# Performance work log

Hardware: AMD Instinct MI355X
Metric: run time of the kernel (lower is better)

## Reference

```python
import jax, jax.numpy as jnp
import numpy as np

DIM, N_HEADS, N_KV_HEADS = 2048, 32, 8
HEAD_DIM = DIM // N_HEADS            # 64
KV_REPEAT = N_HEADS // N_KV_HEADS    # 4
ROPE_THETA = 10000.0


def _rope(x, start_pos):
    # x: [B, T, Hx, hd]  (rotate-half / GPT-NeoX style RoPE)
    B, T, Hx, hd = x.shape
    half = hd // 2
    inv_freq = 1.0 / (ROPE_THETA ** (jnp.arange(half, dtype=jnp.float32) / half))
    pos = (start_pos + jnp.arange(T)).astype(jnp.float32)
    ang = pos[:, None] * inv_freq[None, :]            # [T, half]
    cos = jnp.cos(ang)[None, :, None, :]              # [1, T, 1, half]
    sin = jnp.sin(ang)[None, :, None, :]
    x1, x2 = x[..., :half], x[..., half:]
    return jnp.concatenate([x1 * cos - x2 * sin, x1 * sin + x2 * cos], axis=-1).astype(x.dtype)


def setup_inputs() -> dict:
    key = jax.random.key(0)
    ks = jax.random.split(key, 5)
    B, T = 2, 2048
    s = 1.0 / np.sqrt(DIM)
    return {
        "x": jax.random.normal(ks[0], (B, T, DIM), dtype=jnp.float32),
        "Wq": jax.random.normal(ks[1], (DIM, N_HEADS * HEAD_DIM), dtype=jnp.float32) * s,
        "Wk": jax.random.normal(ks[2], (DIM, N_KV_HEADS * HEAD_DIM), dtype=jnp.float32) * s,
        "Wv": jax.random.normal(ks[3], (DIM, N_KV_HEADS * HEAD_DIM), dtype=jnp.float32) * s,
        "Wo": jax.random.normal(ks[4], (DIM, DIM), dtype=jnp.float32) * s,
        "start_pos": 0,
    }


def reference(x, Wq, Wk, Wv, Wo, start_pos):
    B, T, _ = x.shape
    G, R, hd = N_KV_HEADS, KV_REPEAT, HEAD_DIM
    # projections -> [B, T, H, hd]
    Q = (x @ Wq).reshape(B, T, N_HEADS, hd)
    K = (x @ Wk).reshape(B, T, G, hd)
    V = (x @ Wv).reshape(B, T, G, hd)
    Q = _rope(Q, start_pos)
    K = _rope(K, start_pos)
    # GQA: group query heads as (G kv-groups, R repeats) matching repeat_interleave order
    Qg = Q.reshape(B, T, G, R, hd)
    scale = 1.0 / jnp.sqrt(jnp.asarray(hd, dtype=Q.dtype))
    scores = jnp.einsum('bqgrd,bkgd->bgrqk', Qg, K) * scale   # [B,G,R,T,T]
    # causal mask (is_causal=True since T > 1)
    causal = jnp.tril(jnp.ones((T, T), dtype=bool))
    scores = jnp.where(causal[None, None, None, :, :], scores, jnp.finfo(scores.dtype).min)
    attn = jax.nn.softmax(scores, axis=-1)
    out = jnp.einsum('bgrqk,bkgd->bqgrd', attn, V).reshape(B, T, DIM)
    y = out @ Wo
    # original also returns (K, V) with heads-first layout [B, G, T, hd]
    return (y, K.transpose(0, 2, 1, 3), V.transpose(0, 2, 1, 3))
```

## Files before the change

kernel.cpp:

```cpp
#include <hip/hip_runtime.h>
#include <hip/hip_bf16.h>
#include <stdint.h>


typedef __attribute__((ext_vector_type(4))) float f32x4;
typedef __attribute__((ext_vector_type(16))) float f32x16;
typedef __attribute__((ext_vector_type(8))) short sfrag;
typedef __attribute__((ext_vector_type(8))) __bf16 bfrag;
typedef __attribute__((ext_vector_type(4))) unsigned int u32x4;
typedef unsigned short u16;

__device__ __forceinline__ f32x4 mfma16(sfrag a, sfrag b, f32x4 c) {
  return __builtin_amdgcn_mfma_f32_16x16x32_bf16(
      __builtin_bit_cast(bfrag, a), __builtin_bit_cast(bfrag, b), c, 0, 0, 0);
}
__device__ __forceinline__ f32x16 mfma32(sfrag a, sfrag b, f32x16 c) {
  return __builtin_amdgcn_mfma_f32_32x32x16_bf16(
      __builtin_bit_cast(bfrag, a), __builtin_bit_cast(bfrag, b), c, 0, 0, 0);
}
__device__ __forceinline__ u16 f2b(float f) {
  return __builtin_bit_cast(u16, (__bf16)f);
}
__device__ __forceinline__ unsigned pack2(float a, float b) {
  return (unsigned)f2b(a) | ((unsigned)f2b(b) << 16);
}
__device__ __forceinline__ void swap32(unsigned& a, unsigned& b) {
  asm("v_permlane32_swap_b32 %0, %1" : "+v"(a), "+v"(b));
}

#define GAS __attribute__((address_space(1)))
#define LAS __attribute__((address_space(3)))
__device__ __forceinline__ void gll16(const void* g, void* l) {
  __builtin_amdgcn_global_load_lds((GAS unsigned int*)g, (LAS unsigned int*)l, 16, 0, 0);
}

__global__ __launch_bounds__(256) void k_convx(const float* __restrict__ X,
                                               u16* __restrict__ Y,
                                               const int* __restrict__ sp,
                                               float2* __restrict__ csn) {
  const int bid = blockIdx.x;
  if (bid < 8192) {
    const int i = (bid * 256 + threadIdx.x) * 4;
    float4 v = *(const float4*)(X + i);
    *(ushort4*)(Y + i) = make_ushort4(f2b(v.x), f2b(v.y), f2b(v.z), f2b(v.w));
  } else {
    const int i = (bid - 8192) * 256 + threadIdx.x;
    const int t = i >> 5, j = i & 31;
    const float freq = powf(10000.0f, -(float)j * (1.0f / 32.0f));
    const float ang = (float)(sp[0] + t) * freq;
    csn[i] = make_float2(cosf(ang), sinf(ang));
  }
}

__global__ __launch_bounds__(256) void k_convTall(const float* __restrict__ Wq,
                                                  const float* __restrict__ Wk,
                                                  const float* __restrict__ Wv,
                                                  const float* __restrict__ Wo,
                                                  u16* __restrict__ Wqkvt,
                                                  u16* __restrict__ Wot) {
  __shared__ float tile[64][65];
  const int bx = blockIdx.x;
  const int k0 = blockIdx.y * 64;
  const float* W; int N, n0; u16* Dst; int nd;
  if (bx < 32)      { W = Wq; N = 2048; n0 = bx * 64;        Dst = Wqkvt; nd = n0; }
  else if (bx < 40) { W = Wk; N = 512;  n0 = (bx - 32) * 64; Dst = Wqkvt; nd = 2048 + n0; }
  else if (bx < 48) { W = Wv; N = 512;  n0 = (bx - 40) * 64; Dst = Wqkvt; nd = 2560 + n0; }
  else              { W = Wo; N = 2048; n0 = (bx - 48) * 64; Dst = Wot;   nd = n0; }
  const int tid = threadIdx.x;
  #pragma unroll
  for (int it = 0; it < 4; ++it) {
    const int idx = it * 256 + tid;
    const int kk = idx >> 4, nq = idx & 15;
    float4 v = *(const float4*)(W + (size_t)(k0 + kk) * N + n0 + nq * 4);
    tile[kk][nq * 4 + 0] = v.x;
    tile[kk][nq * 4 + 1] = v.y;
    tile[kk][nq * 4 + 2] = v.z;
    tile[kk][nq * 4 + 3] = v.w;
  }
  __syncthreads();
  #pragma unroll
  for (int it = 0; it < 4; ++it) {
    const int idx = it * 256 + tid;
    const int nn = idx >> 4, kq = idx & 15;
    ushort4 o;
    o.x = f2b(tile[kq * 4 + 0][nn]);
    o.y = f2b(tile[kq * 4 + 1][nn]);
    o.z = f2b(tile[kq * 4 + 2][nn]);
    o.w = f2b(tile[kq * 4 + 3][nn]);
    *(ushort4*)(Dst + (size_t)(nd + nn) * 2048 + k0 + kq * 4) = o;
  }
}

__global__ __launch_bounds__(512, 2) void k_gemmQKV(const u16* __restrict__ A,
                                                    const u16* __restrict__ Bt,
                                                    int K, int GY,
                                                    const float2* __restrict__ csn,
                                                    u16* __restrict__ Qb,
                                                    u16* __restrict__ Kb,
                                                    float* __restrict__ Kout,
                                                    float* __restrict__ Vout) {
  __shared__ u16 lds[16384];
  char* const L = (char*)&lds[0];
  const int tid = threadIdx.x;
  const int q8 = gridDim.x >> 3;
  const int id2 = (blockIdx.x & 7) * q8 + (blockIdx.x >> 3);
  const int by = id2 % GY, bx = id2 / GY;
  const int wid = tid >> 6, lane = tid & 63;
  const int wm = wid >> 1, wn = wid & 1;
  const int l16 = lane & 15, l4 = lane >> 4;
  const size_t K2 = (size_t)K * 2;
  const char* Ab = (const char*)(A + (size_t)(by * 128) * K);
  const char* Bb = (const char*)(Bt + (size_t)(bx * 128) * K);
  const int NT = K >> 6;

  auto stage = [&](const char* gb, int reg, int t) {
    #pragma unroll
    for (int rd = 0; rd < 2; ++rd) {
      const int p = rd * 8192 + tid * 16;
      const int r = p >> 7;
      const int cb = (p & 127) ^ ((r & 7) << 4);
      gll16(gb + (size_t)r * K2 + (size_t)t * 128 + cb, L + reg + p);
    }
  };

  const int swz = (l16 & 7) << 4;
  const int c0 = (l4 * 16) ^ swz;
  const int c1 = (64 + l4 * 16) ^ swz;
  const int aOff = (wm * 32 + l16) * 128;
  const int bOff = 16384 + (wn * 64 + l16) * 128;

  f32x4 acc[2][4];
  #pragma unroll
  for (int m = 0; m < 2; ++m)
    #pragma unroll
    for (int n = 0; n < 4; ++n) acc[m][n] = f32x4{0.f, 0.f, 0.f, 0.f};

  for (int t = 0; t < NT; ++t) {
    stage(Ab, 0, t);
    stage(Bb, 16384, t);
    __syncthreads();
    sfrag a0[2], a1[2], b0[4], b1[4];
    #pragma unroll
    for (int m = 0; m < 2; ++m) {
      a0[m] = *(const sfrag*)(L + aOff + m * 2048 + c0);
      a1[m] = *(const sfrag*)(L + aOff + m * 2048 + c1);
    }
    #pragma unroll
    for (int n = 0; n < 4; ++n) {
      b0[n] = *(const sfrag*)(L + bOff + n * 2048 + c0);
      b1[n] = *(const sfrag*)(L + bOff + n * 2048 + c1);
    }
    #pragma unroll
    for (int m = 0; m < 2; ++m)
      #pragma unroll
      for (int n = 0; n < 4; ++n) {
        acc[m][n] = mfma16(a0[m], b0[n], acc[m][n]);
        acc[m][n] = mfma16(a1[m], b1[n], acc[m][n]);
      }
    __syncthreads();
  }

  const int head = bx * 2 + wn;
  const int row0 = by * 128 + wm * 32;
  if (head < 40) {
    u16* Lw = (u16*)(L + wid * 4096);
    const float QS = 0.125f * 1.44269504f;
    const bool isQ = head < 32;
    #pragma unroll
    for (int m = 0; m < 2; ++m)
      #pragma unroll
      for (int r = 0; r < 4; ++r) {
        const int tl = m * 16 + l4 * 4 + r;
        const int tg = row0 + tl;
        const int b = tg >> 11, t = tg & 2047;
        #pragma unroll
        for (int n = 0; n < 2; ++n) {
          const int j = n * 16 + l16;
          const float2 cz = csn[t * 32 + j];
          const float x1 = acc[m][n][r], x2 = acc[m][n + 2][r];
          const float o1 = x1 * cz.x - x2 * cz.y;
          const float o2 = x1 * cz.y + x2 * cz.x;
          if (isQ) {
            Lw[tl * 64 + j]      = f2b(o1 * QS);
            Lw[tl * 64 + j + 32] = f2b(o2 * QS);
          } else {
            Lw[tl * 64 + j]      = f2b(o1);
            Lw[tl * 64 + j + 32] = f2b(o2);
            const int g = head - 32;
            const size_t o = (((size_t)b * 8 + g) * 2048 + t) * 64 + j;
            Kout[o] = o1;  Kout[o + 32] = o2;
          }
        }
      }
    __syncthreads();
    u16* dst = isQ ? Qb : Kb;
    const int hh = isQ ? head : (head - 32);
    const int hstride = isQ ? 32 : 8;
    #pragma unroll
    for (int it = 0; it < 4; ++it) {
      const int tl = it * 8 + (lane >> 3);
      const int col = (lane & 7) * 8;
      const u32x4 v = *(const u32x4*)&Lw[tl * 64 + col];
      const int tg = row0 + tl;
      const int b = tg >> 11, t = tg & 2047;
      *(u32x4*)(dst + (((size_t)b * hstride + hh) * 2048 + t) * 64 + col) = v;
    }
  } else {
    const int g = head - 40;
    #pragma unroll
    for (int m = 0; m < 2; ++m)
      #pragma unroll
      for (int r = 0; r < 4; ++r) {
        const int tg = row0 + m * 16 + l4 * 4 + r;
        const int b = tg >> 11, t = tg & 2047;
        const size_t o = (((size_t)b * 8 + g) * 2048 + t) * 64;
        #pragma unroll
        for (int n = 0; n < 4; ++n)
          Vout[o + n * 16 + l16] = acc[m][n][r];
      }
  }
}

__global__ __launch_bounds__(512, 2) void k_gemmOut(const u16* __restrict__ A,
                                                    const u16* __restrict__ Bt,
                                                    float* __restrict__ C,
                                                    int N, int K, int GY) {
  __shared__ u16 lds[16384];
  char* const L = (char*)&lds[0];
  const int tid = threadIdx.x;
  const int q8 = gridDim.x >> 3;
  const int id2 = (blockIdx.x & 7) * q8 + (blockIdx.x >> 3);
  const int by = id2 % GY, bx = id2 / GY;
  const int wid = tid >> 6, lane = tid & 63;
  const int wm = wid >> 2, wn = wid & 3;
  const int l16 = lane & 15, l4 = lane >> 4;
  const size_t K2 = (size_t)K * 2;
  const char* Ab = (const char*)(A + (size_t)(by * 128) * K);
  const char* Bb = (const char*)(Bt + (size_t)(bx * 128) * K);
  const int NT = K >> 6;

  auto stage = [&](const char* gb, int reg, int t) {
    #pragma unroll
    for (int rd = 0; rd < 2; ++rd) {
      const int p = rd * 8192 + tid * 16;
      const int r = p >> 7;
      const int cb = (p & 127) ^ ((r & 7) << 4);
      gll16(gb + (size_t)r * K2 + (size_t)t * 128 + cb, L + reg + p);
    }
  };

  const int swz = (l16 & 7) << 4;
  const int c0 = (l4 * 16) ^ swz;
  const int c1 = (64 + l4 * 16) ^ swz;
  const int aOff = (wm * 64 + l16) * 128;
  const int bOff = 16384 + (wn * 32 + l16) * 128;

  f32x4 acc[4][2];
  #pragma unroll
  for (int m = 0; m < 4; ++m)
    #pragma unroll
    for (int n = 0; n < 2; ++n) acc[m][n] = f32x4{0.f, 0.f, 0.f, 0.f};

  for (int t = 0; t < NT; ++t) {
    stage(Ab, 0, t);
    stage(Bb, 16384, t);
    __syncthreads();
    sfrag a0[4], a1[4], b0[2], b1[2];
    #pragma unroll
    for (int m = 0; m < 4; ++m) {
      a0[m] = *(const sfrag*)(L + aOff + m * 2048 + c0);
      a1[m] = *(const sfrag*)(L + aOff + m * 2048 + c1);
    }
    #pragma unroll
    for (int n = 0; n < 2; ++n) {
      b0[n] = *(const sfrag*)(L + bOff + n * 2048 + c0);
      b1[n] = *(const sfrag*)(L + bOff + n * 2048 + c1);
    }
    #pragma unroll
    for (int m = 0; m < 4; ++m)
      #pragma unroll
      for (int n = 0; n < 2; ++n) {
        acc[m][n] = mfma16(a0[m], b0[n], acc[m][n]);
        acc[m][n] = mfma16(a1[m], b1[n], acc[m][n]);
      }
    __syncthreads();
  }

  float* Cb = C + (size_t)(by * 128 + wm * 64) * N + bx * 128 + wn * 32;
  #pragma unroll
  for (int m = 0; m < 4; ++m)
    #pragma unroll
    for (int n = 0; n < 2; ++n)
      #pragma unroll
      for (int r = 0; r < 4; ++r)
        Cb[(size_t)(m * 16 + l4 * 4 + r) * N + n * 16 + l16] = acc[m][n][r];
}

__global__ __launch_bounds__(256) void k_vtrans(const float* __restrict__ Vout,
                                                u16* __restrict__ Vt) {
  __shared__ float tile[64][65];
  int t0 = blockIdx.x * 64;
  int bg = blockIdx.y;
  const float* src = Vout + (size_t)bg * (2048 * 64);
  #pragma unroll
  for (int p = 0; p < 16; ++p) {
    int idx = p * 256 + threadIdx.x;
    int tt = idx >> 6, d = idx & 63;
    tile[tt][d] = src[(size_t)(t0 + tt) * 64 + d];
  }
  __syncthreads();
  #pragma unroll
  for (int p = 0; p < 16; ++p) {
    int idx = p * 256 + threadIdx.x;
    int d = idx >> 6, tt = idx & 63;
    Vt[((size_t)bg * 64 + d) * 2048 + t0 + tt] = f2b(tile[tt][d]);
  }
}

__device__ __forceinline__ void pv4(const float* p, sfrag v0a, sfrag v0b,
                                    sfrag v1a, sfrag v1b,
                                    f32x16& O0, f32x16& O1, float& l) {
  unsigned w[8];
  #pragma unroll
  for (int j = 0; j < 8; ++j) w[j] = pack2(p[2 * j], p[2 * j + 1]);
  swap32(w[0], w[2]);
  swap32(w[1], w[3]);
  swap32(w[4], w[6]);
  swap32(w[5], w[7]);
  const sfrag pf0 = __builtin_bit_cast(sfrag, u32x4{w[0], w[1], w[2], w[3]});
  const sfrag pf1 = __builtin_bit_cast(sfrag, u32x4{w[4], w[5], w[6], w[7]});
  O0 = mfma32(v0a, pf0, O0);
  O0 = mfma32(v0b, pf1, O0);
  O1 = mfma32(v1a, pf0, O1);
  O1 = mfma32(v1b, pf1, O1);
  float s[8];
  #pragma unroll
  for (int j = 0; j < 8; ++j) s[j] = p[j] + p[j + 8];
  #pragma unroll
  for (int j = 0; j < 4; ++j) s[j] = s[j] + s[j + 4];
  l += (s[0] + s[1]) + (s[2] + s[3]);
}

__device__ __forceinline__ void tile64_l(const u16* __restrict__ buf,
                                         const sfrag* qf, int hi, int l31, int swz,
                                         f32x16& O0, f32x16& O1, float& l) {
  const char* Kl = (const char*)buf;
  const char* Vl = Kl + 8192;
  const int rb = l31 * 128;
  f32x16 Sa = {}, Sb = {};
  #pragma unroll
  for (int ks = 0; ks < 4; ++ks) {
    const int col = (hi * 16 + ks * 32) ^ swz;
    const sfrag ka = *(const sfrag*)(Kl + rb + col);
    const sfrag kb = *(const sfrag*)(Kl + rb + col + 4096);
    Sa = mfma32(ka, qf[ks], Sa);
    Sb = mfma32(kb, qf[ks], Sb);
  }
  float pa[16], pb[16];
  #pragma unroll
  for (int r = 0; r < 16; ++r) {
    pa[r] = __builtin_amdgcn_exp2f(Sa[r]);
    pb[r] = __builtin_amdgcn_exp2f(Sb[r]);
  }
  sfrag v0[4], v1[4];
  #pragma unroll
  for (int s = 0; s < 4; ++s) {
    const int col = (s * 32 + hi * 16) ^ swz;
    v0[s] = *(const sfrag*)(Vl + rb + col);
    v1[s] = *(const sfrag*)(Vl + rb + col + 4096);
  }
  pv4(pa, v0[0], v0[1], v1[0], v1[1], O0, O1, l);
  pv4(pb, v0[2], v0[3], v1[2], v1[3], O0, O1, l);
}

template<bool MASKED>
__device__ __forceinline__ void tile32_l(const u16* __restrict__ buf, int c,
                                         const sfrag* qf, int hi, int l31, int swz,
                                         f32x16& O0, f32x16& O1, float& l) {
  const char* Kl = (const char*)buf;
  const char* Vl = Kl + 8192;
  const int rb = l31 * 128;
  f32x16 S = {};
  #pragma unroll
  for (int ks = 0; ks < 4; ++ks) {
    const int col = (hi * 16 + ks * 32) ^ swz;
    const sfrag k = *(const sfrag*)(Kl + c * 4096 + rb + col);
    S = mfma32(k, qf[ks], S);
  }
  float p[16];
  #pragma unroll
  for (int r = 0; r < 16; ++r) {
    float s = S[r];
    if (MASKED) {
      int kvo = (r & 3) + 8 * (r >> 2) + 4 * hi;
      if (kvo > l31) s = -__builtin_inff();
    }
    p[r] = __builtin_amdgcn_exp2f(s);
  }
  const int colA = (c * 64 + hi * 16) ^ swz;
  const int colB = (c * 64 + 32 + hi * 16) ^ swz;
  const sfrag v0a = *(const sfrag*)(Vl + rb + colA);
  const sfrag v0b = *(const sfrag*)(Vl + rb + colB);
  const sfrag v1a = *(const sfrag*)(Vl + rb + colA + 4096);
  const sfrag v1b = *(const sfrag*)(Vl + rb + colB + 4096);
  pv4(p, v0a, v0b, v1a, v1b, O0, O1, l);
}

__global__ __launch_bounds__(256, 2) void k_attn7(const u16* __restrict__ Qb,
                                                  const u16* __restrict__ Kb,
                                                  const u16* __restrict__ Vt,
                                                  u16* __restrict__ attOut) {
  __shared__ u16 lds[2][8192];
  const int bid = blockIdx.x;
  const int qb2 = 31 - (bid >> 4);
  const int bg = bid & 15;
  const int b = bg >> 3, g = bg & 7;
  const int wave = threadIdx.x >> 6, lane = threadIdx.x & 63;
  const int h = g * 4 + wave;
  const int hi = lane >> 5, l31 = lane & 31;
  const int qrow0 = qb2 * 64;
  const int swz = (l31 & 7) << 4;

  const u16* Qp0 = Qb + (((size_t)b * 32 + h) * 2048 + qrow0 + l31) * 64 + hi * 8;
  sfrag qf0[4], qf1[4];
  #pragma unroll
  for (int ks = 0; ks < 4; ++ks) {
    qf0[ks] = *(const sfrag*)(Qp0 + ks * 16);
    qf1[ks] = *(const sfrag*)(Qp0 + 32 * 64 + ks * 16);
  }

  const char* Kg = (const char*)(Kb + ((size_t)b * 8 + g) * (2048 * 64));
  const char* Vg = (const char*)(Vt + ((size_t)b * 8 + g) * (64 * 2048));

  auto stage = [&](int bufi, int t) {
    const char* Ktile = Kg + (size_t)t * 8192;
    const char* Vtile = Vg + t * 128;
    #pragma unroll
    for (int rd = 0; rd < 2; ++rd) {
      const int p = rd * 4096 + threadIdx.x * 16;
      const int d = p >> 7;
      const int cb = (p & 127) ^ ((d & 7) << 4);
      const int lbase = rd * 4096 + wave * 1024;
      gll16(Ktile + d * 128 + cb, (char*)&lds[bufi][0] + lbase);
      gll16(Vtile + (size_t)d * 4096 + cb, (char*)&lds[bufi][0] + 8192 + lbase);
    }
  };

  f32x16 O00 = {}, O01 = {}, O10 = {}, O11 = {};
  float ls0 = 0.f, ls1 = 0.f;
  const int nfull = qb2;
  int cur = 0;
  stage(0, 0);
  for (int t = 0; t < nfull; ++t) {
    __syncthreads();
    stage(cur ^ 1, t + 1);
    tile64_l(lds[cur], qf0, hi, l31, swz, O00, O01, ls0);
    tile64_l(lds[cur], qf1, hi, l31, swz, O10, O11, ls1);
    cur ^= 1;
  }
  __syncthreads();
  tile32_l<true >(lds[cur], 0, qf0, hi, l31, swz, O00, O01, ls0);
  tile32_l<false>(lds[cur], 0, qf1, hi, l31, swz, O10, O11, ls1);
  tile32_l<true >(lds[cur], 1, qf1, hi, l31, swz, O10, O11, ls1);

  #pragma unroll
  for (int sb = 0; sb < 2; ++sb) {
    const float lsum = sb ? ls1 : ls0;
    const float ltot = lsum + __shfl_xor(lsum, 32);
    const float inv = 1.0f / ltot;
    const size_t orow = ((size_t)b * 2048 + qrow0 + sb * 32 + l31) * 2048 + h * 64;
    #pragma unroll
    for (int dt = 0; dt < 2; ++dt) {
      const f32x16& O = sb ? (dt ? O11 : O10) : (dt ? O01 : O00);
      #pragma unroll
      for (int k = 0; k < 4; ++k) {
        ushort4 o;
        o.x = f2b(O[4 * k + 0] * inv);
        o.y = f2b(O[4 * k + 1] * inv);
        o.z = f2b(O[4 * k + 2] * inv);
        o.w = f2b(O[4 * k + 3] * inv);
        *(ushort4*)&attOut[orow + dt * 32 + 8 * k + 4 * hi] = o;
      }
    }
  }
}

extern "C" void kernel_launch(void* const* d_in, const int* in_sizes, int n_in,
                              void* d_out, int out_size, void* d_ws, size_t ws_size,
                              hipStream_t stream) {
  const float* x  = (const float*)d_in[0];
  const float* Wq = (const float*)d_in[1];
  const float* Wk = (const float*)d_in[2];
  const float* Wv = (const float*)d_in[3];
  const float* Wo = (const float*)d_in[4];
  const int* sp   = (const int*)d_in[5];
  float* y    = (float*)d_out;
  float* Kout = y + 8388608;
  float* Vout = y + 10485760;

  char* ws = (char*)d_ws;
  u16*    xb     = (u16*)(ws + 0);
  u16*    Wqkvt  = (u16*)(ws + 16777216);
  u16*    Wot    = (u16*)(ws + 29360128);
  float2* csn    = (float2*)(ws + 37748736);
  u16*    Qbuf   = (u16*)(ws + 88080384);
  u16*    Kbuf   = (u16*)(ws + 104857600);
  u16*    Vt     = (u16*)(ws + 109051904);
  u16*    attOut = xb;

  k_convx<<<8448, 256, 0, stream>>>(x, xb, sp, csn);
  k_convTall<<<dim3(80, 32), 256, 0, stream>>>(Wq, Wk, Wv, Wo, Wqkvt, Wot);
  k_gemmQKV<<<768, 512, 0, stream>>>(xb, Wqkvt, 2048, 32, csn, Qbuf, Kbuf, Kout, Vout);
  k_vtrans<<<dim3(32, 16), 256, 0, stream>>>(Vout, Vt);
  k_attn7<<<512, 256, 0, stream>>>(Qbuf, Kbuf, Vt, attOut);
  k_gemmOut<<<512, 512, 0, stream>>>(attOut, Wot, y, 2048, 2048, 32);
}
```

Before: 176.3 us.

## Fuse V transpose into QKV GEMM epilogue and double K-tile depth

Removes the separate k_vtrans kernel by having the QKV GEMM's V-head blocks transpose their bf16 outputs through LDS and write Vt directly. Both GEMMs now stage 128-wide K tiles (64KB LDS) instead of 64, halving the number of barrier-separated iterations. The larger LDS footprint may limit occupancy to fewer blocks per CU.

```diff
diff --git a/kernel.cpp b/kernel.cpp
--- a/kernel.cpp
+++ b/kernel.cpp
@@ -98,8 +98,9 @@
                                                     u16* __restrict__ Qb,
                                                     u16* __restrict__ Kb,
                                                     float* __restrict__ Kout,
-                                                    float* __restrict__ Vout) {
-  __shared__ u16 lds[16384];
+                                                    float* __restrict__ Vout,
+                                                    u16* __restrict__ Vt) {
+  __shared__ u16 lds[32768];
   char* const L = (char*)&lds[0];
   const int tid = threadIdx.x;
   const int q8 = gridDim.x >> 3;
@@ -111,23 +112,21 @@
   const size_t K2 = (size_t)K * 2;
   const char* Ab = (const char*)(A + (size_t)(by * 128) * K);
   const char* Bb = (const char*)(Bt + (size_t)(bx * 128) * K);
-  const int NT = K >> 6;
+  const int NT = K >> 7;
 
   auto stage = [&](const char* gb, int reg, int t) {
     #pragma unroll
-    for (int rd = 0; rd < 2; ++rd) {
+    for (int rd = 0; rd < 4; ++rd) {
       const int p = rd * 8192 + tid * 16;
-      const int r = p >> 7;
-      const int cb = (p & 127) ^ ((r & 7) << 4);
-      gll16(gb + (size_t)r * K2 + (size_t)t * 128 + cb, L + reg + p);
+      const int r = p >> 8;
+      const int cb = (p & 255) ^ ((r & 7) << 4);
+      gll16(gb + (size_t)r * K2 + (size_t)t * 256 + cb, L + reg + p);
     }
   };
 
   const int swz = (l16 & 7) << 4;
-  const int c0 = (l4 * 16) ^ swz;
-  const int c1 = (64 + l4 * 16) ^ swz;
-  const int aOff = (wm * 32 + l16) * 128;
-  const int bOff = 16384 + (wn * 64 + l16) * 128;
+  const int aOff = (wm * 32 + l16) * 256;
+  const int bOff = 32768 + (wn * 64 + l16) * 256;
 
   f32x4 acc[2][4];
   #pragma unroll
@@ -137,26 +136,24 @@
 
   for (int t = 0; t < NT; ++t) {
     stage(Ab, 0, t);
-    stage(Bb, 16384, t);
-    __syncthreads();
-    sfrag a0[2], a1[2], b0[4], b1[4];
-    #pragma unroll
-    for (int m = 0; m < 2; ++m) {
-      a0[m] = *(const sfrag*)(L + aOff + m * 2048 + c0);
-      a1[m] = *(const sfrag*)(L + aOff + m * 2048 + c1);
-    }
-    #pragma unroll
-    for (int n = 0; n < 4; ++n) {
-      b0[n] = *(const sfrag*)(L + bOff + n * 2048 + c0);
-      b1[n] = *(const sfrag*)(L + bOff + n * 2048 + c1);
-    }
-    #pragma unroll
-    for (int m = 0; m < 2; ++m)
-      #pragma unroll
-      for (int n = 0; n < 4; ++n) {
-        acc[m][n] = mfma16(a0[m], b0[n], acc[m][n]);
-        acc[m][n] = mfma16(a1[m], b1[n], acc[m][n]);
-      }
+    stage(Bb, 32768, t);
+    __syncthreads();
+    #pragma unroll
+    for (int kq = 0; kq < 4; ++kq) {
+      const int ck = (kq * 64 + l4 * 16) ^ swz;
+      sfrag a[2], b[4];
+      #pragma unroll
+      for (int m = 0; m < 2; ++m)
+        a[m] = *(const sfrag*)(L + aOff + m * 4096 + ck);
+      #pragma unroll
+      for (int n = 0; n < 4; ++n)
+        b[n] = *(const sfrag*)(L + bOff + n * 4096 + ck);
+      #pragma unroll
+      for (int m = 0; m < 2; ++m)
+        #pragma unroll
+        for (int n = 0; n < 4; ++n)
+          acc[m][n] = mfma16(a[m], b[n], acc[m][n]);
+    }
     __syncthreads();
   }
 
@@ -207,17 +204,30 @@
     }
   } else {
     const int g = head - 40;
+    u16* Lw = (u16*)(L + wid * 4096);
     #pragma unroll
     for (int m = 0; m < 2; ++m)
       #pragma unroll
       for (int r = 0; r < 4; ++r) {
-        const int tg = row0 + m * 16 + l4 * 4 + r;
+        const int tl = m * 16 + l4 * 4 + r;
+        const int tg = row0 + tl;
         const int b = tg >> 11, t = tg & 2047;
         const size_t o = (((size_t)b * 8 + g) * 2048 + t) * 64;
         #pragma unroll
-        for (int n = 0; n < 4; ++n)
+        for (int n = 0; n < 4; ++n) {
           Vout[o + n * 16 + l16] = acc[m][n][r];
+          Lw[(n * 16 + l16) * 32 + tl] = f2b(acc[m][n][r]);
+        }
       }
+    __syncthreads();
+    const int bb = row0 >> 11, tt0 = row0 & 2047;
+    #pragma unroll
+    for (int it = 0; it < 4; ++it) {
+      const int d = it * 16 + (lane >> 2);
+      const int toff = (lane & 3) * 8;
+      const u32x4 v = *(const u32x4*)&Lw[d * 32 + toff];
+      *(u32x4*)(Vt + (((size_t)bb * 8 + g) * 64 + d) * 2048 + tt0 + toff) = v;
+    }
   }
 }
 
@@ -225,7 +235,7 @@
                                                     const u16* __restrict__ Bt,
                                                     float* __restrict__ C,
                                                     int N, int K, int GY) {
-  __shared__ u16 lds[16384];
+  __shared__ u16 lds[32768];
   char* const L = (char*)&lds[0];
   const int tid = threadIdx.x;
   const int q8 = gridDim.x >> 3;
@@ -237,23 +247,21 @@
   const size_t K2 = (size_t)K * 2;
   const char* Ab = (const char*)(A + (size_t)(by * 128) * K);
   const char* Bb = (const char*)(Bt + (size_t)(bx * 128) * K);
-  const int NT = K >> 6;
+  const int NT = K >> 7;
 
   auto stage = [&](const char* gb, int reg, int t) {
     #pragma unroll
-    for (int rd = 0; rd < 2; ++rd) {
+    for (int rd = 0; rd < 4; ++rd) {
       const int p = rd * 8192 + tid * 16;
-      const int r = p >> 7;
-      const int cb = (p & 127) ^ ((r & 7) << 4);
-      gll16(gb + (size_t)r * K2 + (size_t)t * 128 + cb, L + reg + p);
+      const int r = p >> 8;
+      const int cb = (p & 255) ^ ((r & 7) << 4);
+      gll16(gb + (size_t)r * K2 + (size_t)t * 256 + cb, L + reg + p);
     }
   };
 
   const int swz = (l16 & 7) << 4;
-  const int c0 = (l4 * 16) ^ swz;
-  const int c1 = (64 + l4 * 16) ^ swz;
-  const int aOff = (wm * 64 + l16) * 128;
-  const int bOff = 16384 + (wn * 32 + l16) * 128;
+  const int aOff = (wm * 64 + l16) * 256;
+  const int bOff = 32768 + (wn * 32 + l16) * 256;
 
   f32x4 acc[4][2];
   #pragma unroll
@@ -263,26 +271,24 @@
 
   for (int t = 0; t < NT; ++t) {
     stage(Ab, 0, t);
-    stage(Bb, 16384, t);
-    __syncthreads();
-    sfrag a0[4], a1[4], b0[2], b1[2];
-    #pragma unroll
-    for (int m = 0; m < 4; ++m) {
-      a0[m] = *(const sfrag*)(L + aOff + m * 2048 + c0);
-      a1[m] = *(const sfrag*)(L + aOff + m * 2048 + c1);
-    }
-    #pragma unroll
-    for (int n = 0; n < 2; ++n) {
-      b0[n] = *(const sfrag*)(L + bOff + n * 2048 + c0);
-      b1[n] = *(const sfrag*)(L + bOff + n * 2048 + c1);
-    }
-    #pragma unroll
-    for (int m = 0; m < 4; ++m)
-      #pragma unroll
-      for (int n = 0; n < 2; ++n) {
-        acc[m][n] = mfma16(a0[m], b0[n], acc[m][n]);
-        acc[m][n] = mfma16(a1[m], b1[n], acc[m][n]);
-      }
+    stage(Bb, 32768, t);
+    __syncthreads();
+    #pragma unroll
+    for (int kq = 0; kq < 4; ++kq) {
+      const int ck = (kq * 64 + l4 * 16) ^ swz;
+      sfrag a[4], b[2];
+      #pragma unroll
+      for (int m = 0; m < 4; ++m)
+        a[m] = *(const sfrag*)(L + aOff + m * 4096 + ck);
+      #pragma unroll
+      for (int n = 0; n < 2; ++n)
+        b[n] = *(const sfrag*)(L + bOff + n * 4096 + ck);
+      #pragma unroll
+      for (int m = 0; m < 4; ++m)
+        #pragma unroll
+        for (int n = 0; n < 2; ++n)
+          acc[m][n] = mfma16(a[m], b[n], acc[m][n]);
+    }
     __syncthreads();
   }
 
@@ -294,27 +300,6 @@
       #pragma unroll
       for (int r = 0; r < 4; ++r)
         Cb[(size_t)(m * 16 + l4 * 4 + r) * N + n * 16 + l16] = acc[m][n][r];
-}
-
-__global__ __launch_bounds__(256) void k_vtrans(const float* __restrict__ Vout,
-                                                u16* __restrict__ Vt) {
-  __shared__ float tile[64][65];
-  int t0 = blockIdx.x * 64;
-  int bg = blockIdx.y;
-  const float* src = Vout + (size_t)bg * (2048 * 64);
-  #pragma unroll
-  for (int p = 0; p < 16; ++p) {
-    int idx = p * 256 + threadIdx.x;
-    int tt = idx >> 6, d = idx & 63;
-    tile[tt][d] = src[(size_t)(t0 + tt) * 64 + d];
-  }
-  __syncthreads();
-  #pragma unroll
-  for (int p = 0; p < 16; ++p) {
-    int idx = p * 256 + threadIdx.x;
-    int d = idx >> 6, tt = idx & 63;
-    Vt[((size_t)bg * 64 + d) * 2048 + t0 + tt] = f2b(tile[tt][d]);
-  }
 }
 
 __device__ __forceinline__ void pv4(const float* p, sfrag v0a, sfrag v0b,
@@ -510,8 +495,8 @@
 
   k_convx<<<8448, 256, 0, stream>>>(x, xb, sp, csn);
   k_convTall<<<dim3(80, 32), 256, 0, stream>>>(Wq, Wk, Wv, Wo, Wqkvt, Wot);
-  k_gemmQKV<<<768, 512, 0, stream>>>(xb, Wqkvt, 2048, 32, csn, Qbuf, Kbuf, Kout, Vout);
-  k_vtrans<<<dim3(32, 16), 256, 0, stream>>>(Vout, Vt);
+  k_gemmQKV<<<768, 512, 0, stream>>>(xb, Wqkvt, 2048, 32, csn, Qbuf, Kbuf,
+                                     Kout, Vout, Vt);
   k_attn7<<<512, 256, 0, stream>>>(Qbuf, Kbuf, Vt, attOut);
   k_gemmOut<<<512, 512, 0, stream>>>(attOut, Wot, y, 2048, 2048, 32);
 }
```

New measurement: 191.7 us. 1.09x slower.
